# Kernel optimization log

Measured on AMD Instinct MI355X. Metric: run time of the kernel, lower is better.

Reference implementation:

```python
import jax, jax.numpy as jnp
import numpy as np

NUM_EXPERTS = 16
TOP_K = 2
AUX_LOSS_COEF = 0.01


def setup_inputs() -> dict:
    key = jax.random.key(0)
    ks = jax.random.split(key, 5)
    B, S, D, I, E = 4, 2048, 1024, 2816, NUM_EXPERTS
    scale = 0.02
    return {
        "x": jax.random.normal(ks[0], (B, S, D), dtype=jnp.float32),
        "gate_w": jax.random.normal(ks[1], (D, E), dtype=jnp.float32) * scale,
        "Wg": jax.random.normal(ks[2], (E, D, I), dtype=jnp.float32) * scale,
        "Wu": jax.random.normal(ks[3], (E, D, I), dtype=jnp.float32) * scale,
        "Wd": jax.random.normal(ks[4], (E, I, D), dtype=jnp.float32) * scale,
    }


def _moe_forward(x, gate_w, Wg, Wu, Wd):
    B, S, D = x.shape
    E = gate_w.shape[1]
    # Router
    logits = x @ gate_w                      # [B,S,E]
    probs = jax.nn.softmax(logits, axis=-1)  # [B,S,E]
    topk_w, topk_idx = jax.lax.top_k(probs, TOP_K)        # [B,S,K]
    topk_w = topk_w / jnp.sum(topk_w, axis=-1, keepdims=True)
    # Per-token combine weight for each expert: [B,S,E]
    onehot = jax.nn.one_hot(topk_idx, E, dtype=x.dtype)   # [B,S,K,E]
    combine_w = jnp.einsum("bsk,bske->bse", topk_w, onehot)
    x_flat = x.reshape(-1, D)                # [T,D]
    w_flat = combine_w.reshape(-1, E)        # [T,E]
    # Accumulate weighted expert outputs (loop over fixed small E; unselected
    # tokens get zero weight, identical math to masked gather/scatter).
    out = jnp.zeros_like(x_flat)
    for e in range(E):
        h = jax.nn.silu(x_flat @ Wg[e]) * (x_flat @ Wu[e])  # [T,I]
        out = out + (h @ Wd[e]) * w_flat[:, e:e + 1]
    out = out.reshape(B, S, D)
    # Load balancing aux loss
    expert_mask = onehot.sum(axis=2)                        # [B,S,E]
    tokens_per_expert = expert_mask.mean(axis=(0, 1))       # [E]
    router_prob_per_expert = probs.mean(axis=(0, 1))        # [E]
    aux_loss = AUX_LOSS_COEF * jnp.sum(tokens_per_expert * router_prob_per_expert) * E
    return out, aux_loss


def reference(x, gate_w, Wg, Wu, Wd):
    return _moe_forward(x, gate_w, Wg, Wu, Wd)
```

## Files before the change

### kernel.cpp

```cpp
#include <hip/hip_runtime.h>
#include <stdint.h>

#define T_TOKENS 8192
#define D_DIM 1024
#define I_DIM 2816
#define E_NUM 16
#define N_SLOTS 16384

typedef float f32x4 __attribute__((ext_vector_type(4)));
typedef short s16x8 __attribute__((ext_vector_type(8)));
typedef short s16x4 __attribute__((ext_vector_type(4)));
typedef unsigned short u16;
typedef unsigned int u32;

__device__ __forceinline__ u16 f2bf(float f) {
  u32 u = __builtin_bit_cast(u32, f);
  u = (u + 0x7FFFu + ((u >> 16) & 1u)) >> 16;
  return (u16)u;
}
__device__ __forceinline__ u32 pack2(float a, float b) {
  return (u32)f2bf(a) | ((u32)f2bf(b) << 16);
}
__device__ __forceinline__ void async_load16(const void* g, void* l) {
  __builtin_amdgcn_global_load_lds(
      (const __attribute__((address_space(1))) void*)g,
      (__attribute__((address_space(3))) void*)l, 16, 0, 0);
}

__global__ void router_kernel(const float* __restrict__ x,
                              const float* __restrict__ gw,
                              int* __restrict__ e12, float* __restrict__ w12,
                              int* __restrict__ cnt, float* __restrict__ probsum) {
  __shared__ float sProb[E_NUM];
  __shared__ int sCnt[E_NUM];
  int tid = threadIdx.x;
  if (tid < E_NUM) { sProb[tid] = 0.f; sCnt[tid] = 0; }
  __syncthreads();
  int g = tid >> 4, i = tid & 15;
  int t = blockIdx.x * 16 + g;
  float acc[E_NUM];
#pragma unroll
  for (int e = 0; e < E_NUM; e++) acc[e] = 0.f;
  const f32x4* x4 = (const f32x4*)(x + (size_t)t * D_DIM);
  const f32x4* g4 = (const f32x4*)gw;
  for (int jj = 0; jj < 16; jj++) {
    f32x4 xv = x4[i + 16 * jj];
    int jb = 4 * (i + 16 * jj);
#pragma unroll
    for (int r = 0; r < 4; r++) {
      float xs = xv[r];
#pragma unroll
      for (int e4 = 0; e4 < 4; e4++) {
        f32x4 gv = g4[(jb + r) * 4 + e4];
        acc[e4 * 4 + 0] += xs * gv[0];
        acc[e4 * 4 + 1] += xs * gv[1];
        acc[e4 * 4 + 2] += xs * gv[2];
        acc[e4 * 4 + 3] += xs * gv[3];
      }
    }
  }
#pragma unroll
  for (int e = 0; e < E_NUM; e++) {
    float v = acc[e];
    v += __shfl_down(v, 8, 16);
    v += __shfl_down(v, 4, 16);
    v += __shfl_down(v, 2, 16);
    v += __shfl_down(v, 1, 16);
    acc[e] = v;
  }
  if (i == 0) {
    float mx = acc[0];
#pragma unroll
    for (int e = 1; e < E_NUM; e++) mx = fmaxf(mx, acc[e]);
    float p[E_NUM]; float s = 0.f;
#pragma unroll
    for (int e = 0; e < E_NUM; e++) { p[e] = __expf(acc[e] - mx); s += p[e]; }
    float inv = 1.f / s;
#pragma unroll
    for (int e = 0; e < E_NUM; e++) p[e] *= inv;
    int e1 = 0; float p1 = p[0];
#pragma unroll
    for (int e = 1; e < E_NUM; e++) if (p[e] > p1) { p1 = p[e]; e1 = e; }
    int e2 = (e1 == 0) ? 1 : 0; float p2 = p[e2];
#pragma unroll
    for (int e = 0; e < E_NUM; e++) if (e != e1 && p[e] > p2) { p2 = p[e]; e2 = e; }
    float wsum = p1 + p2;
    e12[2 * t] = e1; e12[2 * t + 1] = e2;
    w12[2 * t] = p1 / wsum; w12[2 * t + 1] = p2 / wsum;
#pragma unroll
    for (int e = 0; e < E_NUM; e++) atomicAdd(&sProb[e], p[e]);
    atomicAdd(&sCnt[e1], 1);
    atomicAdd(&sCnt[e2], 1);
  }
  __syncthreads();
  if (tid < E_NUM) {
    atomicAdd(&cnt[tid], sCnt[tid]);
    atomicAdd(&probsum[tid], sProb[tid]);
  }
}

__global__ void prefix_kernel(const int* __restrict__ cnt, int* __restrict__ offsets,
                              const float* __restrict__ probsum, float* __restrict__ aux_out) {
  if (threadIdx.x == 0) {
    int s = 0;
    for (int e = 0; e < E_NUM; e++) { offsets[e] = s; s += cnt[e]; }
    offsets[E_NUM] = s;
    float a = 0.f;
    for (int e = 0; e < E_NUM; e++) a += (float)cnt[e] * probsum[e];
    aux_out[0] = 0.01f * 16.f * a / (8192.f * 8192.f);
  }
}

__global__ void build_kernel(const int* __restrict__ e12, const float* __restrict__ w12,
                             const int* __restrict__ offsets, int* __restrict__ cursor,
                             int* __restrict__ tlist, float* __restrict__ wlist,
                             int* __restrict__ slot2) {
  int t = blockIdx.x * 256 + threadIdx.x;
  if (t >= T_TOKENS) return;
#pragma unroll
  for (int k = 0; k < 2; k++) {
    int e = e12[2 * t + k];
    int pos = atomicAdd(&cursor[e], 1);
    int idx = offsets[e] + pos;
    tlist[idx] = t;
    wlist[idx] = w12[2 * t + k];
    slot2[2 * t + k] = idx;
  }
}

__global__ void gather_kernel(const float* __restrict__ x, const int* __restrict__ tlist,
                              u16* __restrict__ Xe) {
  int r = blockIdx.x * 4 + (threadIdx.x >> 6);
  int lane = threadIdx.x & 63;
  int tok = tlist[r];
  const f32x4* src = (const f32x4*)(x + (size_t)tok * D_DIM);
  u32* dst = (u32*)(Xe + (size_t)r * D_DIM);
#pragma unroll
  for (int c = 0; c < 4; c++) {
    f32x4 v = src[lane + 64 * c];
    dst[(lane + 64 * c) * 2] = pack2(v[0], v[1]);
    dst[(lane + 64 * c) * 2 + 1] = pack2(v[2], v[3]);
  }
}

template <int K, int N>
__global__ __launch_bounds__(256) void transpose_kernel(const float* __restrict__ W,
                                                        u16* __restrict__ Wt) {
  __shared__ u16 tile[64][258];
  int e = blockIdx.z;
  int k0 = blockIdx.x * 64;
  int n0 = blockIdx.y * 256;
  const float* Win = W + (size_t)e * K * N;
  u16* Wout = Wt + (size_t)e * N * K;
  int t = threadIdx.x;
  int r = t >> 4;
  int c4 = (t & 15) * 4;
#pragma unroll
  for (int rep = 0; rep < 4; rep++) {
    int k = r + rep * 16;
    const float* rowp = Win + (size_t)(k0 + k) * N + n0;
#pragma unroll
    for (int s = 0; s < 4; s++) {
      f32x4 v = *(const f32x4*)(rowp + s * 64 + c4);
      *(u32*)&tile[k][s * 64 + c4] = pack2(v[0], v[1]);
      *(u32*)&tile[k][s * 64 + c4 + 2] = pack2(v[2], v[3]);
    }
  }
  __syncthreads();
#pragma unroll
  for (int rep = 0; rep < 8; rep++) {
    int c = t + 256 * rep;
    int n = c >> 3;
    int k8 = (c & 7) * 8;
    s16x8 o;
#pragma unroll
    for (int i = 0; i < 8; i++) o[i] = tile[k8 + i][n];
    *(s16x8*)(Wout + (size_t)(n0 + n) * K + k0 + k8) = o;
  }
}

__global__ __launch_bounds__(256, 2) void gemm_gu_kernel(
    const u16* __restrict__ Abuf, const u16* __restrict__ Bg, const u16* __restrict__ Bu,
    u16* __restrict__ Hbuf,
    const int* __restrict__ cnt, const int* __restrict__ offsets) {
  int e = blockIdx.z;
  int Me = cnt[e];
  int m0 = blockIdx.y * 128;
  if (m0 >= Me) return;
  int n0 = blockIdx.x * 128;
  int rowBase = offsets[e];
  const u16* Bge = Bg + (size_t)e * I_DIM * D_DIM;
  const u16* Bue = Bu + (size_t)e * I_DIM * D_DIM;

  __shared__ u16 Ash[128 * 64];
  __shared__ u16 Bgsh[128 * 64];
  __shared__ u16 Bush[128 * 64];

  int tid = threadIdx.x;
  int lane = tid & 63;
  int wv = tid >> 6;
  int wm = wv >> 1;
  int wn = wv & 1;
  int lrow = lane & 15, lq = lane >> 4;
  int swz = lrow & 7;

  f32x4 accg[4][4], accu[4][4];
#pragma unroll
  for (int a = 0; a < 4; a++)
#pragma unroll
    for (int b = 0; b < 4; b++) { accg[a][b] = (f32x4)0.f; accu[a][b] = (f32x4)0.f; }

  for (int kt = 0; kt < 16; kt++) {
    int k0 = kt << 6;
#pragma unroll
    for (int r = 0; r < 4; r++) {
      int c = tid + 256 * r;
      int row = c >> 3, slot = c & 7;
      int co = (slot ^ (row & 7)) << 3;
      int ldso = (wv * 64 + 256 * r) * 8;
      int gr = m0 + row; gr = (gr < Me) ? gr : (Me - 1);
      async_load16(Abuf + (size_t)(rowBase + gr) * D_DIM + k0 + co, &Ash[ldso]);
      async_load16(Bge + (size_t)(n0 + row) * D_DIM + k0 + co, &Bgsh[ldso]);
      async_load16(Bue + (size_t)(n0 + row) * D_DIM + k0 + co, &Bush[ldso]);
    }
    __syncthreads();
#pragma unroll
    for (int kh = 0; kh < 2; kh++) {
      s16x8 af[4], bg[4], bu[4];
      int so = ((kh * 4 + lq) ^ swz) << 3;
#pragma unroll
      for (int f = 0; f < 4; f++) {
        af[f] = *(const s16x8*)&Ash[(wm * 64 + f * 16 + lrow) * 64 + so];
        bg[f] = *(const s16x8*)&Bgsh[(wn * 64 + f * 16 + lrow) * 64 + so];
        bu[f] = *(const s16x8*)&Bush[(wn * 64 + f * 16 + lrow) * 64 + so];
      }
#pragma unroll
      for (int fm = 0; fm < 4; fm++)
#pragma unroll
        for (int fn = 0; fn < 4; fn++) {
          accg[fm][fn] = __builtin_amdgcn_mfma_f32_16x16x32_bf16(af[fm], bg[fn], accg[fm][fn], 0, 0, 0);
          accu[fm][fn] = __builtin_amdgcn_mfma_f32_16x16x32_bf16(af[fm], bu[fn], accu[fm][fn], 0, 0, 0);
        }
    }
    __syncthreads();
  }

#pragma unroll
  for (int fm = 0; fm < 4; fm++) {
#pragma unroll
    for (int i = 0; i < 4; i++) {
      int m = m0 + wm * 64 + fm * 16 + lq * 4 + i;
      if (m >= Me) continue;
      size_t arow = (size_t)(rowBase + m);
#pragma unroll
      for (int fn = 0; fn < 4; fn++) {
        int col = n0 + wn * 64 + fn * 16 + lrow;
        float g = accg[fm][fn][i];
        float u = accu[fm][fn][i];
        float h = (g / (1.f + __expf(-g))) * u;
        Hbuf[arow * I_DIM + col] = f2bf(h);
      }
    }
  }
}

__global__ __launch_bounds__(256, 3) void gemm_down_kernel(
    const u16* __restrict__ Abuf, const u16* __restrict__ Bd, float* __restrict__ Y,
    const int* __restrict__ cnt, const int* __restrict__ offsets,
    const float* __restrict__ wlist) {
  int e = blockIdx.z;
  int Me = cnt[e];
  int m0 = blockIdx.y * 128;
  if (m0 >= Me) return;
  int n0 = blockIdx.x * 128;
  int rowBase = offsets[e];
  const u16* Bde = Bd + (size_t)e * D_DIM * I_DIM;

  __shared__ u16 Ash[128 * 64];
  __shared__ u16 Bsh[128 * 64];

  int tid = threadIdx.x;
  int lane = tid & 63;
  int wv = tid >> 6;
  int wm = wv >> 1;
  int wn = wv & 1;
  int lrow = lane & 15, lq = lane >> 4;
  int swz = lrow & 7;

  f32x4 acc[4][4];
#pragma unroll
  for (int a = 0; a < 4; a++)
#pragma unroll
    for (int b = 0; b < 4; b++) acc[a][b] = (f32x4)0.f;

  for (int kt = 0; kt < 44; kt++) {
    int k0 = kt << 6;
#pragma unroll
    for (int r = 0; r < 4; r++) {
      int c = tid + 256 * r;
      int row = c >> 3, slot = c & 7;
      int co = (slot ^ (row & 7)) << 3;
      int ldso = (wv * 64 + 256 * r) * 8;
      int gr = m0 + row; gr = (gr < Me) ? gr : (Me - 1);
      async_load16(Abuf + (size_t)(rowBase + gr) * I_DIM + k0 + co, &Ash[ldso]);
      async_load16(Bde + (size_t)(n0 + row) * I_DIM + k0 + co, &Bsh[ldso]);
    }
    __syncthreads();
#pragma unroll
    for (int kh = 0; kh < 2; kh++) {
      s16x8 af[4], bb[4];
      int so = ((kh * 4 + lq) ^ swz) << 3;
#pragma unroll
      for (int f = 0; f < 4; f++) {
        af[f] = *(const s16x8*)&Ash[(wm * 64 + f * 16 + lrow) * 64 + so];
        bb[f] = *(const s16x8*)&Bsh[(wn * 64 + f * 16 + lrow) * 64 + so];
      }
#pragma unroll
      for (int fm = 0; fm < 4; fm++)
#pragma unroll
        for (int fn = 0; fn < 4; fn++)
          acc[fm][fn] = __builtin_amdgcn_mfma_f32_16x16x32_bf16(af[fm], bb[fn], acc[fm][fn], 0, 0, 0);
    }
    __syncthreads();
  }

#pragma unroll
  for (int fm = 0; fm < 4; fm++) {
#pragma unroll
    for (int i = 0; i < 4; i++) {
      int m = m0 + wm * 64 + fm * 16 + lq * 4 + i;
      if (m >= Me) continue;
      size_t arow = (size_t)(rowBase + m);
      float w = wlist[arow];
#pragma unroll
      for (int fn = 0; fn < 4; fn++) {
        int col = n0 + wn * 64 + fn * 16 + lrow;
        Y[arow * D_DIM + col] = acc[fm][fn][i] * w;
      }
    }
  }
}

__global__ __launch_bounds__(256) void combine_kernel(
    const float* __restrict__ Y, const int* __restrict__ slot2,
    float* __restrict__ out) {
  int t = blockIdx.x;
  int tid = threadIdx.x;
  int s1 = slot2[2 * t];
  int s2 = slot2[2 * t + 1];
  const f32x4* y1 = (const f32x4*)(Y + (size_t)s1 * D_DIM);
  const f32x4* y2 = (const f32x4*)(Y + (size_t)s2 * D_DIM);
  f32x4* o = (f32x4*)(out + (size_t)t * D_DIM);
  o[tid] = y1[tid] + y2[tid];
}

extern "C" void kernel_launch(void* const* d_in, const int* in_sizes, int n_in,
                              void* d_out, int out_size, void* d_ws, size_t ws_size,
                              hipStream_t stream) {
  const float* x  = (const float*)d_in[0];
  const float* gw = (const float*)d_in[1];
  const float* Wg = (const float*)d_in[2];
  const float* Wu = (const float*)d_in[3];
  const float* Wd = (const float*)d_in[4];
  float* outf = (float*)d_out;
  char* ws = (char*)d_ws;
  int*   cnt     = (int*)(ws + 0);
  int*   cursor  = (int*)(ws + 64);
  float* probsum = (float*)(ws + 128);
  int*   offsets = (int*)(ws + 192);
  int*   e12     = (int*)(ws + 512);
  float* w12     = (float*)(ws + 66048);
  int*   tlist   = (int*)(ws + 131584);
  float* wlist   = (float*)(ws + 197120);
  int*   slot2   = (int*)(ws + 262656);
  u16*   Xe      = (u16*)(ws + (1 << 20));
  u16*   H       = (u16*)(ws + 34603008);
  u16*   WtA     = (u16*)(ws + 134217728);
  u16*   WtB     = (u16*)(ws + 234881024);
  float* Y       = (float*)(ws + 234881024);

  hipMemsetAsync(d_ws, 0, 512, stream);

  router_kernel<<<512, 256, 0, stream>>>(x, gw, e12, w12, cnt, probsum);
  prefix_kernel<<<1, 64, 0, stream>>>(cnt, offsets, probsum, outf + (size_t)(T_TOKENS * D_DIM));
  build_kernel<<<32, 256, 0, stream>>>(e12, w12, offsets, cursor, tlist, wlist, slot2);
  gather_kernel<<<4096, 256, 0, stream>>>(x, tlist, Xe);

  transpose_kernel<D_DIM, I_DIM><<<dim3(16, 11, E_NUM), 256, 0, stream>>>(Wg, WtA);
  transpose_kernel<D_DIM, I_DIM><<<dim3(16, 11, E_NUM), 256, 0, stream>>>(Wu, WtB);

  gemm_gu_kernel<<<dim3(22, 64, E_NUM), 256, 0, stream>>>(Xe, WtA, WtB, H, cnt, offsets);

  transpose_kernel<I_DIM, D_DIM><<<dim3(44, 4, E_NUM), 256, 0, stream>>>(Wd, WtA);

  gemm_down_kernel<<<dim3(8, 64, E_NUM), 256, 0, stream>>>(H, WtA, Y, cnt, offsets, wlist);

  combine_kernel<<<T_TOKENS, 256, 0, stream>>>(Y, slot2, outf);
}
```

Baseline: 1.090 ms.

## Merge gate/up weight transposes, swap GU grid order, widen down-proj N tile

The gate and up weight transposes now run as a single launch with a doubled z grid, which saves one launch and its tail. The gate/up GEMM grid now maps blockIdx.x to M tiles and blockIdx.y to N tiles. Early-exiting blocks for empty M tiles of an expert are therefore adjacent in dispatch order, which may also change L2 reuse of weight tiles. The down GEMM tile grows from 128x128 to 128x256 with 8 N fragments per wave and occupancy lowered to 2 blocks. That halves re-reads of the A (H) tiles but raises register and LDS pressure and cuts the number of blocks.

After: 1.562 ms. 1.43x slower.

```diff
diff --git a/kernel.cpp b/kernel.cpp
--- a/kernel.cpp
+++ b/kernel.cpp
@@ -144,10 +144,15 @@
 }
 
 template <int K, int N>
-__global__ __launch_bounds__(256) void transpose_kernel(const float* __restrict__ W,
-                                                        u16* __restrict__ Wt) {
+__global__ __launch_bounds__(256) void transpose2_kernel(const float* __restrict__ W0,
+                                                         const float* __restrict__ W1,
+                                                         u16* __restrict__ O0,
+                                                         u16* __restrict__ O1) {
   __shared__ u16 tile[64][258];
-  int e = blockIdx.z;
+  int zz = blockIdx.z;
+  int e = zz & (E_NUM - 1);
+  const float* W = (zz < E_NUM) ? W0 : W1;
+  u16* Wt = (zz < E_NUM) ? O0 : O1;
   int k0 = blockIdx.x * 64;
   int n0 = blockIdx.y * 256;
   const float* Win = W + (size_t)e * K * N;
@@ -185,9 +190,9 @@
     const int* __restrict__ cnt, const int* __restrict__ offsets) {
   int e = blockIdx.z;
   int Me = cnt[e];
-  int m0 = blockIdx.y * 128;
+  int m0 = blockIdx.x * 128;
   if (m0 >= Me) return;
-  int n0 = blockIdx.x * 128;
+  int n0 = blockIdx.y * 128;
   int rowBase = offsets[e];
   const u16* Bge = Bg + (size_t)e * I_DIM * D_DIM;
   const u16* Bue = Bu + (size_t)e * I_DIM * D_DIM;
@@ -264,7 +269,7 @@
   }
 }
 
-__global__ __launch_bounds__(256, 3) void gemm_down_kernel(
+__global__ __launch_bounds__(256, 2) void gemm_down_kernel(
     const u16* __restrict__ Abuf, const u16* __restrict__ Bd, float* __restrict__ Y,
     const int* __restrict__ cnt, const int* __restrict__ offsets,
     const float* __restrict__ wlist) {
@@ -272,12 +277,12 @@
   int Me = cnt[e];
   int m0 = blockIdx.y * 128;
   if (m0 >= Me) return;
-  int n0 = blockIdx.x * 128;
+  int n0 = blockIdx.x * 256;
   int rowBase = offsets[e];
   const u16* Bde = Bd + (size_t)e * D_DIM * I_DIM;
 
   __shared__ u16 Ash[128 * 64];
-  __shared__ u16 Bsh[128 * 64];
+  __shared__ u16 Bsh[256 * 64];
 
   int tid = threadIdx.x;
   int lane = tid & 63;
@@ -287,11 +292,11 @@
   int lrow = lane & 15, lq = lane >> 4;
   int swz = lrow & 7;
 
-  f32x4 acc[4][4];
+  f32x4 acc[4][8];
 #pragma unroll
   for (int a = 0; a < 4; a++)
 #pragma unroll
-    for (int b = 0; b < 4; b++) acc[a][b] = (f32x4)0.f;
+    for (int b = 0; b < 8; b++) acc[a][b] = (f32x4)0.f;
 
   for (int kt = 0; kt < 44; kt++) {
     int k0 = kt << 6;
@@ -303,22 +308,30 @@
       int ldso = (wv * 64 + 256 * r) * 8;
       int gr = m0 + row; gr = (gr < Me) ? gr : (Me - 1);
       async_load16(Abuf + (size_t)(rowBase + gr) * I_DIM + k0 + co, &Ash[ldso]);
+    }
+#pragma unroll
+    for (int r = 0; r < 8; r++) {
+      int c = tid + 256 * r;
+      int row = c >> 3, slot = c & 7;
+      int co = (slot ^ (row & 7)) << 3;
+      int ldso = (wv * 64 + 256 * r) * 8;
       async_load16(Bde + (size_t)(n0 + row) * I_DIM + k0 + co, &Bsh[ldso]);
     }
     __syncthreads();
 #pragma unroll
     for (int kh = 0; kh < 2; kh++) {
-      s16x8 af[4], bb[4];
+      s16x8 af[4], bb[8];
       int so = ((kh * 4 + lq) ^ swz) << 3;
 #pragma unroll
-      for (int f = 0; f < 4; f++) {
+      for (int f = 0; f < 4; f++)
         af[f] = *(const s16x8*)&Ash[(wm * 64 + f * 16 + lrow) * 64 + so];
-        bb[f] = *(const s16x8*)&Bsh[(wn * 64 + f * 16 + lrow) * 64 + so];
-      }
+#pragma unroll
+      for (int fn = 0; fn < 8; fn++)
+        bb[fn] = *(const s16x8*)&Bsh[(wn * 128 + fn * 16 + lrow) * 64 + so];
 #pragma unroll
       for (int fm = 0; fm < 4; fm++)
 #pragma unroll
-        for (int fn = 0; fn < 4; fn++)
+        for (int fn = 0; fn < 8; fn++)
           acc[fm][fn] = __builtin_amdgcn_mfma_f32_16x16x32_bf16(af[fm], bb[fn], acc[fm][fn], 0, 0, 0);
     }
     __syncthreads();
@@ -333,8 +346,8 @@
       size_t arow = (size_t)(rowBase + m);
       float w = wlist[arow];
 #pragma unroll
-      for (int fn = 0; fn < 4; fn++) {
-        int col = n0 + wn * 64 + fn * 16 + lrow;
+      for (int fn = 0; fn < 8; fn++) {
+        int col = n0 + wn * 128 + fn * 16 + lrow;
         Y[arow * D_DIM + col] = acc[fm][fn][i] * w;
       }
     }
@@ -386,14 +399,13 @@
   build_kernel<<<32, 256, 0, stream>>>(e12, w12, offsets, cursor, tlist, wlist, slot2);
   gather_kernel<<<4096, 256, 0, stream>>>(x, tlist, Xe);
 
-  transpose_kernel<D_DIM, I_DIM><<<dim3(16, 11, E_NUM), 256, 0, stream>>>(Wg, WtA);
-  transpose_kernel<D_DIM, I_DIM><<<dim3(16, 11, E_NUM), 256, 0, stream>>>(Wu, WtB);
-
-  gemm_gu_kernel<<<dim3(22, 64, E_NUM), 256, 0, stream>>>(Xe, WtA, WtB, H, cnt, offsets);
-
-  transpose_kernel<I_DIM, D_DIM><<<dim3(44, 4, E_NUM), 256, 0, stream>>>(Wd, WtA);
-
-  gemm_down_kernel<<<dim3(8, 64, E_NUM), 256, 0, stream>>>(H, WtA, Y, cnt, offsets, wlist);
+  transpose2_kernel<D_DIM, I_DIM><<<dim3(16, 11, 2 * E_NUM), 256, 0, stream>>>(Wg, Wu, WtA, WtB);
+
+  gemm_gu_kernel<<<dim3(64, 22, E_NUM), 256, 0, stream>>>(Xe, WtA, WtB, H, cnt, offsets);
+
+  transpose2_kernel<I_DIM, D_DIM><<<dim3(44, 4, E_NUM), 256, 0, stream>>>(Wd, Wd, WtA, WtA);
+
+  gemm_down_kernel<<<dim3(4, 64, E_NUM), 256, 0, stream>>>(H, WtA, Y, cnt, offsets, wlist);
 
   combine_kernel<<<T_TOKENS, 256, 0, stream>>>(Y, slot2, outf);
 }
```
